# Optimization experiments

Measured on AMD Instinct MI355X. Metric: run time of the kernel, lower is better.

## Reference

```python
import jax, jax.numpy as jnp
import numpy as np

NUM_EMBEDDINGS = 512
EMBEDDING_DIM = 128
COMMITMENT_COST = 0.6
MID_HR = 100.0
HR_RANGE = 70.0


def setup_inputs() -> dict:
    key = jax.random.key(0)
    k1, k2 = jax.random.split(key)
    inputs = jax.random.normal(k1, (64, 2048, EMBEDDING_DIM), dtype=jnp.float32)
    # torch init: uniform(-1/K, 1/K)
    emb_weight = jax.random.uniform(
        k2, (NUM_EMBEDDINGS, EMBEDDING_DIM), dtype=jnp.float32,
        minval=-1.0 / NUM_EMBEDDINGS, maxval=1.0 / NUM_EMBEDDINGS)
    scaling = jnp.ones((NUM_EMBEDDINGS,), dtype=jnp.float32)
    return {"inputs": inputs, "emb_weight": emb_weight, "scaling": scaling}


def reference(inputs, emb_weight, scaling):
    B, T, D = inputs.shape
    K = emb_weight.shape[0]
    flat = inputs.reshape(-1, D)  # [N, D]
    # squared L2 distances to all codes: [N, K]
    distances = (
        jnp.sum(flat * flat, axis=1, keepdims=True)
        + jnp.sum(emb_weight * emb_weight, axis=1)
        - 2.0 * flat @ emb_weight.T
    )
    hr_values = jnp.linspace(40.0, 180.0, K, dtype=jnp.float32)
    hr_weights = 1.0 + scaling * ((hr_values - MID_HR) / HR_RANGE)  # [K]
    encoding_indices = jnp.argmin(distances * hr_weights[None, :], axis=1)  # [N]
    # one-hot @ codebook == direct gather
    quantized = emb_weight[encoding_indices].reshape(inputs.shape)
    e_latent_loss = jnp.mean((jax.lax.stop_gradient(quantized) - inputs) ** 2)
    q_latent_loss = jnp.mean((quantized - jax.lax.stop_gradient(inputs)) ** 2)
    loss = q_latent_loss + COMMITMENT_COST * e_latent_loss
    # straight-through estimator
    quantized_st = inputs + jax.lax.stop_gradient(quantized - inputs)
    return quantized_st, loss, encoding_indices.reshape(B, T)
```

## Files before the change

kernel.cpp:

```cpp
#include <hip/hip_runtime.h>

#define NCODES 512
#define DIM 128
#define NROWS (64*2048)
#define QN (NROWS*DIM)
#define BLK_ROWS 128
#define NBLOCKS (NROWS/BLK_ROWS)
#define NWAVES 8

typedef __attribute__((ext_vector_type(4))) float f32x4;

#define GLOAD_LDS16(gp, lp) __builtin_amdgcn_global_load_lds( \
    (__attribute__((address_space(1))) void*)(gp), \
    (__attribute__((address_space(3))) void*)(lp), 16, 0, 0)

__global__ void vq_prep(const float* __restrict__ emb, const float* __restrict__ scaling,
                        unsigned char* __restrict__ e8frag,
                        float* __restrict__ wv, float* __restrict__ wse,
                        float* __restrict__ wrcp) {
  int k = blockIdx.x;
  int l = threadIdx.x;
  float2 v = ((const float2*)(emb + k * DIM))[l];
  float ss = v.x * v.x + v.y * v.y;
#pragma unroll
  for (int m = 1; m < 64; m <<= 1) ss += __shfl_xor(ss, m);
  int p = __builtin_amdgcn_cvt_pk_fp8_f32(v.x * 512.0f, v.y * 512.0f, 0, false);
  int t = k >> 4, col = k & 15;
  int c = l >> 4, g = (l >> 2) & 3, jp = l & 3;
  *(unsigned short*)(e8frag + (((t * 4 + c) * 64 + g * 16 + col) << 3) + 2 * jp) =
      (unsigned short)(p & 0xFFFF);
  if (l == 0) {
    float hr = 40.0f + (float)k * (140.0f / 511.0f);
    float wt = 1.0f + scaling[k] * ((hr - 100.0f) * (1.0f / 70.0f));
    wv[k] = wt;
    wse[k] = wt * ss;
    wrcp[k] = 1.0f / wt;
  }
}

struct SmemT {
  unsigned char frag[NCODES * DIM];
  float w[NCODES];
  float wse[NCODES];
  float wrcp[NCODES];
  float lossp[NWAVES];
};

__global__ __launch_bounds__(512, 4) void vq_main(
    const float* __restrict__ x,
    const float* __restrict__ emb32,
    const unsigned char* __restrict__ e8frag,
    const float* __restrict__ wv,
    const float* __restrict__ wse,
    const float* __restrict__ wrcp,
    float* __restrict__ out_q,
    float* __restrict__ out_idx,
    float* __restrict__ out_loss) {
  __shared__ SmemT sm;
  const int tid = threadIdx.x;
  const int wave = tid >> 6, lane = tid & 63;
  const int g = lane >> 4, lr = lane & 15;
  const long rowbase = (long)blockIdx.x * BLK_ROWS + wave * 16;

  float4 xv[4][2];
  {
    const float* xr = x + (rowbase + lr) * DIM + g * 8;
#pragma unroll
    for (int c = 0; c < 4; c++) {
      xv[c][0] = *(const float4*)(xr + c * 32);
      xv[c][1] = *(const float4*)(xr + c * 32 + 4);
    }
  }

  {
#pragma unroll
    for (int i = 0; i < 8; i++) {
      int slot = i * 512 + tid;
      GLOAD_LDS16(e8frag + slot * 16, sm.frag + slot * 16);
    }
    sm.w[tid] = wv[tid]; sm.wse[tid] = wse[tid]; sm.wrcp[tid] = wrcp[tid];
  }

  long a[4];
  float sr[4];
  {
    float ss = 0.f;
#pragma unroll
    for (int c = 0; c < 4; c++) {
      float4 v0 = xv[c][0];
      float4 v1 = xv[c][1];
      ss += v0.x * v0.x + v0.y * v0.y + v0.z * v0.z + v0.w * v0.w;
      ss += v1.x * v1.x + v1.y * v1.y + v1.z * v1.z + v1.w * v1.w;
      int lo = __builtin_amdgcn_cvt_pk_fp8_f32(v0.x, v0.y, 0, false);
      lo = __builtin_amdgcn_cvt_pk_fp8_f32(v0.z, v0.w, lo, true);
      int hi = __builtin_amdgcn_cvt_pk_fp8_f32(v1.x, v1.y, 0, false);
      hi = __builtin_amdgcn_cvt_pk_fp8_f32(v1.z, v1.w, hi, true);
      a[c] = (long)(((unsigned long long)(unsigned)hi << 32) |
                    (unsigned long long)(unsigned)lo);
    }
    ss += __shfl_xor(ss, 16);
    ss += __shfl_xor(ss, 32);
#pragma unroll
    for (int r = 0; r < 4; r++)
      sr[r] = __shfl(ss, g * 4 + r);
  }
  __syncthreads();

  unsigned pmin[4];
#pragma unroll
  for (int r = 0; r < 4; r++) pmin[r] = 0xFFFFFFFFu;

  const long* __restrict__ bbase = (const long*)sm.frag + lane;
#pragma unroll 2
  for (int t = 0; t < 32; t++) {
    const unsigned code = t * 16 + lr;
    const float wt = sm.w[code];
    const float bb = sm.wse[code];
    const float m2w = -2.0f * wt * (1.0f / 512.0f);
    f32x4 acc = {0.f, 0.f, 0.f, 0.f};
#pragma unroll
    for (int c = 0; c < 4; c++) {
      long bf = bbase[(t * 4 + c) * 64];
      acc = __builtin_amdgcn_mfma_f32_16x16x32_fp8_fp8(a[c], bf, acc, 0, 0, 0);
    }
#pragma unroll
    for (int r = 0; r < 4; r++) {
      float v = fmaf(m2w, acc[r], fmaf(wt, sr[r], bb));
      unsigned u = (__builtin_bit_cast(unsigned, v) & 0xFFFFFE00u) | code;
      pmin[r] = min(pmin[r], u);
    }
  }

#pragma unroll
  for (int m = 1; m <= 8; m <<= 1) {
#pragma unroll
    for (int r = 0; r < 4; r++) {
      unsigned o = (unsigned)__shfl_xor((int)pmin[r], m);
      pmin[r] = min(pmin[r], o);
    }
  }

  const uint4* __restrict__ esrc = (const uint4*)emb32;
  uint4* __restrict__ outu = (uint4*)out_q + rowbase * 32;
  const int col = lane & 31;
  const int hi2 = lane >> 5;
  int scode[8];
#pragma unroll
  for (int it = 0; it < 8; it++) {
    const int row0 = 2 * it;
    int c0 = __shfl((int)pmin[row0 & 3], (row0 >> 2) * 16);
    int c1 = __shfl((int)pmin[(row0 + 1) & 3], ((row0 + 1) >> 2) * 16);
    scode[it] = (hi2 ? c1 : c0) & 511;
  }

  uint4 vbuf[8];
#pragma unroll
  for (int j = 0; j < 8; j++)
    vbuf[j] = esrc[scode[j] * 32 + col];

  {
    float l0 = 0.f;
#pragma unroll
    for (int r = 0; r < 4; r++) {
      unsigned wn = pmin[r];
      int ci = (int)(wn & 511u);
      float dist = __builtin_bit_cast(float, wn & 0xFFFFFE00u);
      l0 = fmaf(dist, sm.wrcp[ci], l0);
      if (lr == 0) out_idx[rowbase + g * 4 + r] = (float)ci;
    }
    l0 += __shfl_xor(l0, 16);
    l0 += __shfl_xor(l0, 32);
    if (lane == 0) sm.lossp[wave] = l0;
  }

#pragma unroll
  for (int j = 0; j < 8; j++)
    outu[j * 64 + lane] = vbuf[j];

  __syncthreads();
  if (wave == 0 && lane < NWAVES) {
    float s = sm.lossp[lane];
#pragma unroll
    for (int m = 1; m < NWAVES; m <<= 1) s += __shfl_xor(s, m);
    if (lane == 0) atomicAdd(out_loss, s * (1.6f / (float)QN));
  }
}

extern "C" void kernel_launch(void* const* d_in, const int* in_sizes, int n_in,
                              void* d_out, int out_size, void* d_ws, size_t ws_size,
                              hipStream_t stream) {
  const float* x = (const float*)d_in[0];
  const float* emb = (const float*)d_in[1];
  const float* scaling = (const float*)d_in[2];

  float* out_q = (float*)d_out;
  float* out_loss = out_q + QN;
  float* out_idx = out_q + QN + 1;

  unsigned char* e8frag = (unsigned char*)d_ws;
  float* wv = (float*)((char*)d_ws + NCODES * DIM);
  float* wse = wv + NCODES;
  float* wrcp = wse + NCODES;

  hipMemsetAsync(out_loss, 0, sizeof(float), stream);
  vq_prep<<<NCODES, 64, 0, stream>>>(emb, scaling, e8frag, wv, wse, wrcp);
  vq_main<<<NBLOCKS, 512, 0, stream>>>(x, emb, e8frag, wv, wse, wrcp,
                                       out_q, out_idx, out_loss);
}
```

Before: 44.75 us.

## Replace FP8 MFMA distance search with norm-bound screening and exact fallback

Drops the FP8 MFMA search over all codes. Instead, each lane owns a row, computes a Cauchy-Schwarz lower bound on the weighted distance to every code from norms alone, keeps the best two, and verifies the winner exactly in FP32. If the second bound does not clear the exact winner distance, the lane falls back to a full scalar FP32 search over all codes. This aims to remove the matmul work but risks heavy divergent fallback loops when the bounds are not tight. It also changes block size and output write layout.

New measurement: 71.79 us. +60.4%, slower.

```diff
diff --git a/kernel.cpp b/kernel.cpp
--- a/kernel.cpp
+++ b/kernel.cpp
@@ -4,184 +4,154 @@
 #define DIM 128
 #define NROWS (64*2048)
 #define QN (NROWS*DIM)
-#define BLK_ROWS 128
+#define BLK_ROWS 256
 #define NBLOCKS (NROWS/BLK_ROWS)
-#define NWAVES 8
+#define NWAVES 4
 
-typedef __attribute__((ext_vector_type(4))) float f32x4;
-
-#define GLOAD_LDS16(gp, lp) __builtin_amdgcn_global_load_lds( \
-    (__attribute__((address_space(1))) void*)(gp), \
-    (__attribute__((address_space(3))) void*)(lp), 16, 0, 0)
+__device__ __forceinline__ unsigned umin_(unsigned a, unsigned b) { return a < b ? a : b; }
+__device__ __forceinline__ unsigned umax_(unsigned a, unsigned b) { return a > b ? a : b; }
 
 __global__ void vq_prep(const float* __restrict__ emb, const float* __restrict__ scaling,
-                        unsigned char* __restrict__ e8frag,
-                        float* __restrict__ wv, float* __restrict__ wse,
-                        float* __restrict__ wrcp) {
+                        float* __restrict__ wv, float* __restrict__ ssv,
+                        float* __restrict__ betav, float* __restrict__ gammav) {
   int k = blockIdx.x;
   int l = threadIdx.x;
   float2 v = ((const float2*)(emb + k * DIM))[l];
   float ss = v.x * v.x + v.y * v.y;
 #pragma unroll
   for (int m = 1; m < 64; m <<= 1) ss += __shfl_xor(ss, m);
-  int p = __builtin_amdgcn_cvt_pk_fp8_f32(v.x * 512.0f, v.y * 512.0f, 0, false);
-  int t = k >> 4, col = k & 15;
-  int c = l >> 4, g = (l >> 2) & 3, jp = l & 3;
-  *(unsigned short*)(e8frag + (((t * 4 + c) * 64 + g * 16 + col) << 3) + 2 * jp) =
-      (unsigned short)(p & 0xFFFF);
   if (l == 0) {
     float hr = 40.0f + (float)k * (140.0f / 511.0f);
     float wt = 1.0f + scaling[k] * ((hr - 100.0f) * (1.0f / 70.0f));
     wv[k] = wt;
-    wse[k] = wt * ss;
-    wrcp[k] = 1.0f / wt;
+    ssv[k] = ss;
+    betav[k] = wt * ss;
+    gammav[k] = 2.0f * fabsf(wt) * sqrtf(ss) * (1.0f + 1e-4f);
   }
 }
 
-struct SmemT {
-  unsigned char frag[NCODES * DIM];
-  float w[NCODES];
-  float wse[NCODES];
-  float wrcp[NCODES];
-  float lossp[NWAVES];
-};
-
-__global__ __launch_bounds__(512, 4) void vq_main(
+__global__ __launch_bounds__(256, 4) void vq_main(
     const float* __restrict__ x,
     const float* __restrict__ emb32,
-    const unsigned char* __restrict__ e8frag,
     const float* __restrict__ wv,
-    const float* __restrict__ wse,
-    const float* __restrict__ wrcp,
+    const float* __restrict__ ssv,
+    const float* __restrict__ betav,
+    const float* __restrict__ gammav,
     float* __restrict__ out_q,
     float* __restrict__ out_idx,
     float* __restrict__ out_loss) {
-  __shared__ SmemT sm;
+  __shared__ float lossp[NWAVES];
   const int tid = threadIdx.x;
   const int wave = tid >> 6, lane = tid & 63;
-  const int g = lane >> 4, lr = lane & 15;
-  const long rowbase = (long)blockIdx.x * BLK_ROWS + wave * 16;
+  const int q8 = lane >> 3, c8 = lane & 7;
+  const long rowW = (long)blockIdx.x * BLK_ROWS + wave * 64;
 
-  float4 xv[4][2];
-  {
-    const float* xr = x + (rowbase + lr) * DIM + g * 8;
+  float S = 0.f;
 #pragma unroll
-    for (int c = 0; c < 4; c++) {
-      xv[c][0] = *(const float4*)(xr + c * 32);
-      xv[c][1] = *(const float4*)(xr + c * 32 + 4);
+  for (int it = 0; it < 8; ++it) {
+    const float4* xr = (const float4*)(x + (rowW + it * 8 + q8) * DIM + c8 * 16);
+    float4 a = xr[0], b = xr[1], c = xr[2], d = xr[3];
+    float ssp = a.x*a.x + a.y*a.y + a.z*a.z + a.w*a.w
+              + b.x*b.x + b.y*b.y + b.z*b.z + b.w*b.w
+              + c.x*c.x + c.y*c.y + c.z*c.z + c.w*c.w
+              + d.x*d.x + d.y*d.y + d.z*d.z + d.w*d.w;
+    ssp += __shfl_xor(ssp, 1);
+    ssp += __shfl_xor(ssp, 2);
+    ssp += __shfl_xor(ssp, 4);
+    float got = __shfl(ssp, (lane & 7) << 3);
+    if (q8 == it) S = got;
+  }
+  const float xn = sqrtf(S);
+
+  unsigned m1 = 0xFFFFFFFFu, m2 = 0xFFFFFFFFu;
+#pragma unroll 16
+  for (int k = 0; k < NCODES; ++k) {
+    float w = wv[k], be = betav[k], ga = gammav[k];
+    float L = fmaf(-ga, xn, fmaf(w, S, be));
+    unsigned u = (__builtin_bit_cast(unsigned, L) & 0xFFFFFE00u) | (unsigned)k;
+    unsigned mx = umax_(m1, u);
+    m2 = umin_(m2, mx);
+    m1 = umin_(m1, u);
+  }
+  const int kb = (int)(m1 & 511u);
+  const float ssb = ssv[kb], wb = wv[kb];
+
+  float D = 0.f, dW = 0.f;
+#pragma unroll
+  for (int it = 0; it < 8; ++it) {
+    const int srcl = it * 8 + q8;
+    const int kr = __shfl(kb, srcl);
+    const float4* xr = (const float4*)(x + (rowW + it * 8 + q8) * DIM + c8 * 16);
+    const float4* er = (const float4*)(emb32 + kr * DIM + c8 * 16);
+    float4 xa = xr[0], xb = xr[1], xc = xr[2], xd = xr[3];
+    float4 ea = er[0], eb = er[1], ec = er[2], ed = er[3];
+    float p = 0.f;
+    p = fmaf(xa.x, ea.x, p); p = fmaf(xa.y, ea.y, p);
+    p = fmaf(xa.z, ea.z, p); p = fmaf(xa.w, ea.w, p);
+    p = fmaf(xb.x, eb.x, p); p = fmaf(xb.y, eb.y, p);
+    p = fmaf(xb.z, eb.z, p); p = fmaf(xb.w, eb.w, p);
+    p = fmaf(xc.x, ec.x, p); p = fmaf(xc.y, ec.y, p);
+    p = fmaf(xc.z, ec.z, p); p = fmaf(xc.w, ec.w, p);
+    p = fmaf(xd.x, ed.x, p); p = fmaf(xd.y, ed.y, p);
+    p = fmaf(xd.z, ed.z, p); p = fmaf(xd.w, ed.w, p);
+    p += __shfl_xor(p, 1);
+    p += __shfl_xor(p, 2);
+    p += __shfl_xor(p, 4);
+    float got = __shfl(p, (lane & 7) << 3);
+    if (q8 == it) {
+      D = fmaf(-2.0f, got, S + ssb);
+      dW = wb * D;
     }
   }
 
+  int win = kb;
   {
-#pragma unroll
-    for (int i = 0; i < 8; i++) {
-      int slot = i * 512 + tid;
-      GLOAD_LDS16(e8frag + slot * 16, sm.frag + slot * 16);
-    }
-    sm.w[tid] = wv[tid]; sm.wse[tid] = wse[tid]; sm.wrcp[tid] = wrcp[tid];
-  }
-
-  long a[4];
-  float sr[4];
-  {
-    float ss = 0.f;
-#pragma unroll
-    for (int c = 0; c < 4; c++) {
-      float4 v0 = xv[c][0];
-      float4 v1 = xv[c][1];
-      ss += v0.x * v0.x + v0.y * v0.y + v0.z * v0.z + v0.w * v0.w;
-      ss += v1.x * v1.x + v1.y * v1.y + v1.z * v1.z + v1.w * v1.w;
-      int lo = __builtin_amdgcn_cvt_pk_fp8_f32(v0.x, v0.y, 0, false);
-      lo = __builtin_amdgcn_cvt_pk_fp8_f32(v0.z, v0.w, lo, true);
-      int hi = __builtin_amdgcn_cvt_pk_fp8_f32(v1.x, v1.y, 0, false);
-      hi = __builtin_amdgcn_cvt_pk_fp8_f32(v1.z, v1.w, hi, true);
-      a[c] = (long)(((unsigned long long)(unsigned)hi << 32) |
-                    (unsigned long long)(unsigned)lo);
-    }
-    ss += __shfl_xor(ss, 16);
-    ss += __shfl_xor(ss, 32);
-#pragma unroll
-    for (int r = 0; r < 4; r++)
-      sr[r] = __shfl(ss, g * 4 + r);
-  }
-  __syncthreads();
-
-  unsigned pmin[4];
-#pragma unroll
-  for (int r = 0; r < 4; r++) pmin[r] = 0xFFFFFFFFu;
-
-  const long* __restrict__ bbase = (const long*)sm.frag + lane;
-#pragma unroll 2
-  for (int t = 0; t < 32; t++) {
-    const unsigned code = t * 16 + lr;
-    const float wt = sm.w[code];
-    const float bb = sm.wse[code];
-    const float m2w = -2.0f * wt * (1.0f / 512.0f);
-    f32x4 acc = {0.f, 0.f, 0.f, 0.f};
-#pragma unroll
-    for (int c = 0; c < 4; c++) {
-      long bf = bbase[(t * 4 + c) * 64];
-      acc = __builtin_amdgcn_mfma_f32_16x16x32_fp8_fp8(a[c], bf, acc, 0, 0, 0);
-    }
-#pragma unroll
-    for (int r = 0; r < 4; r++) {
-      float v = fmaf(m2w, acc[r], fmaf(wt, sr[r], bb));
-      unsigned u = (__builtin_bit_cast(unsigned, v) & 0xFFFFFE00u) | code;
-      pmin[r] = min(pmin[r], u);
+    float m2L = __builtin_bit_cast(float, m2 & 0xFFFFFE00u);
+    float thr = fmaf(fabsf(dW), 1e-5f, dW + 1e-6f);
+    if (m2L <= thr) {
+      float bd = 3.4e38f, bD = 0.f;
+      int bi = 0;
+      const float* xr = x + (rowW + lane) * DIM;
+      for (int k = 0; k < NCODES; ++k) {
+        const float* er = emb32 + k * DIM;
+        float p = 0.f;
+        for (int d = 0; d < DIM; ++d) p = fmaf(xr[d], er[d], p);
+        float D2 = S + ssv[k] - 2.0f * p;
+        float dw2 = wv[k] * D2;
+        if (dw2 < bd) { bd = dw2; bi = k; bD = D2; }
+      }
+      win = bi;
+      D = bD;
     }
   }
 
+  out_idx[rowW + lane] = (float)win;
+  {
+    float l0 = D;
 #pragma unroll
-  for (int m = 1; m <= 8; m <<= 1) {
-#pragma unroll
-    for (int r = 0; r < 4; r++) {
-      unsigned o = (unsigned)__shfl_xor((int)pmin[r], m);
-      pmin[r] = min(pmin[r], o);
-    }
-  }
-
-  const uint4* __restrict__ esrc = (const uint4*)emb32;
-  uint4* __restrict__ outu = (uint4*)out_q + rowbase * 32;
-  const int col = lane & 31;
-  const int hi2 = lane >> 5;
-  int scode[8];
-#pragma unroll
-  for (int it = 0; it < 8; it++) {
-    const int row0 = 2 * it;
-    int c0 = __shfl((int)pmin[row0 & 3], (row0 >> 2) * 16);
-    int c1 = __shfl((int)pmin[(row0 + 1) & 3], ((row0 + 1) >> 2) * 16);
-    scode[it] = (hi2 ? c1 : c0) & 511;
-  }
-
-  uint4 vbuf[8];
-#pragma unroll
-  for (int j = 0; j < 8; j++)
-    vbuf[j] = esrc[scode[j] * 32 + col];
-
-  {
-    float l0 = 0.f;
-#pragma unroll
-    for (int r = 0; r < 4; r++) {
-      unsigned wn = pmin[r];
-      int ci = (int)(wn & 511u);
-      float dist = __builtin_bit_cast(float, wn & 0xFFFFFE00u);
-      l0 = fmaf(dist, sm.wrcp[ci], l0);
-      if (lr == 0) out_idx[rowbase + g * 4 + r] = (float)ci;
-    }
-    l0 += __shfl_xor(l0, 16);
-    l0 += __shfl_xor(l0, 32);
-    if (lane == 0) sm.lossp[wave] = l0;
+    for (int m = 1; m < 64; m <<= 1) l0 += __shfl_xor(l0, m);
+    if (lane == 0) lossp[wave] = l0;
   }
 
 #pragma unroll
-  for (int j = 0; j < 8; j++)
-    outu[j * 64 + lane] = vbuf[j];
+  for (int it = 0; it < 8; it += 2) {
+    const int kA = __shfl(win, it * 8 + q8);
+    const int kB = __shfl(win, (it + 1) * 8 + q8);
+    const float4* eA = (const float4*)(emb32 + kA * DIM + c8 * 16);
+    const float4* eB = (const float4*)(emb32 + kB * DIM + c8 * 16);
+    float4 a0 = eA[0], a1 = eA[1], a2 = eA[2], a3 = eA[3];
+    float4 b0 = eB[0], b1 = eB[1], b2 = eB[2], b3 = eB[3];
+    float4* oA = (float4*)(out_q + (rowW + it * 8 + q8) * DIM + c8 * 16);
+    float4* oB = (float4*)(out_q + (rowW + (it + 1) * 8 + q8) * DIM + c8 * 16);
+    oA[0] = a0; oA[1] = a1; oA[2] = a2; oA[3] = a3;
+    oB[0] = b0; oB[1] = b1; oB[2] = b2; oB[3] = b3;
+  }
 
   __syncthreads();
-  if (wave == 0 && lane < NWAVES) {
-    float s = sm.lossp[lane];
-#pragma unroll
-    for (int m = 1; m < NWAVES; m <<= 1) s += __shfl_xor(s, m);
+  if (wave == 0) {
+    float s = (lane < NWAVES) ? lossp[lane] : 0.f;
+    s += __shfl_xor(s, 1);
+    s += __shfl_xor(s, 2);
     if (lane == 0) atomicAdd(out_loss, s * (1.6f / (float)QN));
   }
 }
@@ -197,13 +167,13 @@
   float* out_loss = out_q + QN;
   float* out_idx = out_q + QN + 1;
 
-  unsigned char* e8frag = (unsigned char*)d_ws;
-  float* wv = (float*)((char*)d_ws + NCODES * DIM);
-  float* wse = wv + NCODES;
-  float* wrcp = wse + NCODES;
+  float* wv = (float*)d_ws;
+  float* ssv = wv + NCODES;
+  float* betav = ssv + NCODES;
+  float* gammav = betav + NCODES;
 
   hipMemsetAsync(out_loss, 0, sizeof(float), stream);
-  vq_prep<<<NCODES, 64, 0, stream>>>(emb, scaling, e8frag, wv, wse, wrcp);
-  vq_main<<<NBLOCKS, 512, 0, stream>>>(x, emb, e8frag, wv, wse, wrcp,
+  vq_prep<<<NCODES, 64, 0, stream>>>(emb, scaling, wv, ssv, betav, gammav);
+  vq_main<<<NBLOCKS, 256, 0, stream>>>(x, emb, wv, ssv, betav, gammav,
                                        out_q, out_idx, out_loss);
 }
```
